# Performance work log

Hardware: AMD Instinct MI355X
Metric: run time of the kernel (lower is better)

## Reference

```python
import jax, jax.numpy as jnp
import numpy as np

STRIDE = 1
PAD = 1
KH = KW = 3


def _conv2d(x, w, b, stride, pad):
    out = jax.lax.conv_general_dilated(
        x, w, window_strides=(stride, stride),
        padding=[(pad, pad), (pad, pad)],
        dimension_numbers=("NCHW", "OIHW", "NCHW"))
    return out + b[None, :, None, None]


def _deform_conv2d(x, offset, mask, weight, stride, pad):
    """Modulated deformable conv v2 (torchvision deform_conv2d semantics, no bias).

    x: [B,C,H,W]  offset: [B,2*K2,Ho,Wo] (dy,dx interleaved per tap)
    mask: [B,K2,Ho,Wo]  weight: [O,C,KH,KW]
    """
    B, C, H, W = x.shape
    O = weight.shape[0]
    K2 = KH * KW
    Ho, Wo = offset.shape[2], offset.shape[3]

    dy = offset[:, 0::2]  # [B,K2,Ho,Wo]
    dx = offset[:, 1::2]

    # base sampling grid per kernel tap k = i*KW + j
    ki = jnp.repeat(jnp.arange(KH), KW)  # [K2]
    kj = jnp.tile(jnp.arange(KW), KH)    # [K2]
    base_y = (jnp.arange(Ho) * stride - pad)[None, :, None] + ki[:, None, None]  # [K2,Ho,1]
    base_x = (jnp.arange(Wo) * stride - pad)[None, None, :] + kj[:, None, None]  # [K2,1,Wo]

    py = base_y[None].astype(x.dtype) + dy  # [B,K2,Ho,Wo]
    px = base_x[None].astype(x.dtype) + dx

    y0f = jnp.floor(py)
    x0f = jnp.floor(px)
    wy = py - y0f  # bilinear weights
    wx = px - x0f
    y0 = y0f.astype(jnp.int32)
    x0 = x0f.astype(jnp.int32)

    x_flat = x.reshape(B, C, H * W)

    def gather(yi, xi):
        # zero padding: out-of-range integer neighbors contribute 0
        valid = (yi >= 0) & (yi < H) & (xi >= 0) & (xi < W)
        idx = jnp.clip(yi, 0, H - 1) * W + jnp.clip(xi, 0, W - 1)  # [B,K2,Ho,Wo]
        g = jax.vmap(lambda xf, id_: xf[:, id_])(x_flat, idx)      # [B,C,K2,Ho,Wo]
        return g * valid[:, None].astype(x.dtype)

    v00 = gather(y0, x0)
    v01 = gather(y0, x0 + 1)
    v10 = gather(y0 + 1, x0)
    v11 = gather(y0 + 1, x0 + 1)

    wy_ = wy[:, None]  # [B,1,K2,Ho,Wo]
    wx_ = wx[:, None]
    val = (v00 * (1 - wy_) * (1 - wx_) + v01 * (1 - wy_) * wx_
           + v10 * wy_ * (1 - wx_) + v11 * wy_ * wx_)
    val = val * mask[:, None]

    # conv accumulation over (C, K2)
    return jnp.einsum("bckhw,ock->bohw", val, weight.reshape(O, C, K2))


def setup_inputs() -> dict:
    key = jax.random.key(0)
    ks = jax.random.split(key, 6)
    B, C, O, H, W = 4, 128, 128, 64, 64
    x = jax.random.normal(ks[0], (B, C, H, W), dtype=jnp.float32)
    org_w = jax.random.normal(ks[1], (O, C, KH, KW), dtype=jnp.float32) * 0.05
    offset_w = jax.random.normal(ks[2], (2 * KH * KW, C, 3, 3), dtype=jnp.float32) * 0.01
    offset_b = jax.random.normal(ks[3], (2 * KH * KW,), dtype=jnp.float32) * 0.01
    mask_w = jax.random.normal(ks[4], (KH * KW, C, 3, 3), dtype=jnp.float32) * 0.01
    mask_b = jax.random.normal(ks[5], (KH * KW,), dtype=jnp.float32) * 0.01
    return {"x": x, "org_w": org_w, "offset_w": offset_w, "offset_b": offset_b,
            "mask_w": mask_w, "mask_b": mask_b}


def reference(x, org_w, offset_w, offset_b, mask_w, mask_b):
    offset = _conv2d(x, offset_w, offset_b, STRIDE, 1)          # [B,18,H,W]
    mask = jax.nn.sigmoid(_conv2d(x, mask_w, mask_b, STRIDE, 1))  # [B,9,H,W]
    return _deform_conv2d(x, offset, mask, org_w, STRIDE, PAD)
```

## Files before the change

kernel.cpp:

```cpp
#include <hip/hip_runtime.h>
#include <hip/hip_bf16.h>
#include <cmath>

#define B_    4
#define C_    128
#define O_    128
#define K2T   9
#define CK    1152
#define NPIX  4096
#define ROWS  7
#define BUFC  448
#define BUFV  (16 * BUFC)
#define NGRP  36

using bf16   = __bf16;
using bf16x8 = __attribute__((ext_vector_type(8))) __bf16;
using f32x4  = __attribute__((ext_vector_type(4))) float;

#define WS_WBF 0
#define WS_WOM 294912

__global__ void __launch_bounds__(256) repack_kernel(
    const float* __restrict__ org_w, const float* __restrict__ offset_w,
    const float* __restrict__ mask_w, bf16* __restrict__ w_bf,
    bf16* __restrict__ wom_bf) {
  int t = blockIdx.x * 256 + threadIdx.x;
  if (t >= 160 * CK) return;
  int row = t / CK, r = t % CK;
  int cc = r / 288, rr = r % 288;
  int k = rr >> 5, cq = rr & 31;
  int c = cc * 32 + cq;
  if (row < 128) {
    w_bf[t] = (bf16)org_w[((size_t)row * C_ + c) * K2T + k];
  } else {
    int ch = row - 128;
    float v = 0.f;
    if (ch < 18)      v = offset_w[((size_t)ch * C_ + c) * K2T + k];
    else if (ch < 27) v = mask_w[((size_t)(ch - 18) * C_ + c) * K2T + k];
    wom_bf[(size_t)ch * CK + r] = (bf16)v;
  }
}

__device__ __forceinline__ void gl_lds16(const float* src, float* lds_uniform) {
  __builtin_amdgcn_global_load_lds(
      (const __attribute__((address_space(1))) void*)src,
      (__attribute__((address_space(3))) void*)lds_uniform, 16, 0, 0);
}

__global__ void __launch_bounds__(576) deform_fused_kernel(
    const float* __restrict__ x, const bf16* __restrict__ w_bf,
    const bf16* __restrict__ wom_bf, const float* __restrict__ off_b,
    const float* __restrict__ mask_b, float* __restrict__ out) {
  __shared__ __align__(16) float xslab[4 * BUFV];
  __shared__ __align__(16) bf16  valbuf[NGRP * 512];
  __shared__ __align__(16) float S_lds[32 * 64];

  int tid  = threadIdx.x;
  int bid0 = blockIdx.x;
  int bid  = (bid0 & 7) * 32 + (bid0 >> 3);
  int b    = bid >> 6, ho = bid & 63;
  int lane = tid & 63, wv = tid >> 6;
  int l15  = lane & 15, l4 = lane >> 4;
  bool w8  = (wv < 8);

  const float* xb = x + (size_t)b * C_ * NPIX;

  auto stage = [&](int t) {
    if (w8 && t < 16) {
      int chbase = (t & 7) * 16;
      float* bufb = xslab + (size_t)(t & 3) * BUFV;
#pragma unroll
      for (int u = 0; u < 2; ++u) {
        int chl = 2 * wv + u;
        const float* srcc = xb + (size_t)(chbase + chl) * NPIX + l15 * 4;
        float* dst = bufb + chl * BUFC;
        if (t < 8) {
          int y = ho - 1 + l4; y = y < 0 ? 0 : (y > 63 ? 63 : y);
          gl_lds16(srcc + y * 64, dst + 128);
        } else {
          int ya = ho - 3 + l4; ya = ya < 0 ? 0 : (ya > 63 ? 63 : ya);
          int yb = ho + l4;     yb = yb < 0 ? 0 : (yb > 63 ? 63 : yb);
          gl_lds16(srcc + ya * 64, dst);
          gl_lds16(srcc + yb * 64, dst + 192);
        }
      }
    }
  };

  float apw; int apsa;
  {
    int ki = wv / 3, kj = wv % 3;
    int row = ho - 1 + ki, colu = lane - 1 + kj;
    bool ok = ((unsigned)row < 64u) && ((unsigned)colu < 64u);
    int ccl = colu < 0 ? 0 : (colu > 63 ? 63 : colu);
    apw  = ok ? 1.f : 0.f;
    apsa = (ki + 2) * 64 + ccl;
  }

  stage(0); stage(1); stage(2); stage(3);
  __builtin_amdgcn_sched_barrier(0);

  f32x4 acc1 = {};
  f32x4 acc[4] = {};
  bf16x8 aF[9];
  float pw0 = 0.f, pw1 = 0.f, pw2 = 0.f, pw3 = 0.f;
  int   psa = 0, psb = 0;
  int   mf1 = wv & 1, nfq1 = wv >> 1;
  const bf16* wb1 = wom_bf + (size_t)(mf1 * 16 + l15) * CK + l4 * 8;
  const bf16* wb  = w_bf  + (size_t)(wv * 16 + l15) * CK + l4 * 8;
  const bf16* vr1 = valbuf + l4 * 512 + (nfq1 * 16 + (l15 ^ l4)) * 8;
  const bf16* vrB = valbuf + l4 * 512 + (l15 ^ l4) * 8;

#pragma unroll 1
  for (int p = 0; p < 8; ++p) {
    bool passB = (p >= 4);
    int cc = p & 3;
    if (p == 7)      asm volatile("s_waitcnt vmcnt(0)" ::: "memory");
    else if (p < 3)  asm volatile("s_waitcnt vmcnt(4)" ::: "memory");
    else             asm volatile("s_waitcnt vmcnt(8)" ::: "memory");
    __builtin_amdgcn_s_barrier();
    __builtin_amdgcn_sched_barrier(0);
    if (w8) {
      const bf16* ab = (passB ? wb : wb1) + cc * 288;
#pragma unroll
      for (int ks = 0; ks < 9; ++ks) aF[ks] = *(const bf16x8*)(ab + ks * 32);
      __builtin_amdgcn_sched_barrier(0);
    }
    {
      const float* bufA = xslab + (size_t)((2 * p) & 3) * BUFV;
      const float* bufB2 = xslab + (size_t)((2 * p + 1) & 3) * BUFV;
#pragma unroll
      for (int q = 0; q < 4; ++q) {
        const float* bb = (q < 2) ? bufA : bufB2;
        int h = q & 1;
        bf16x8 pack;
        if (passB) {
#pragma unroll
          for (int j = 0; j < 8; ++j) {
            const float* cb = bb + (h * 8 + j) * BUFC;
            float a0 = cb[psa], a1 = cb[psa + 64];
            float b0 = cb[psb], b1 = cb[psb + 64];
            pack[j] = (bf16)(pw0 * a0 + pw1 * b0 + pw2 * a1 + pw3 * b1);
          }
        } else {
#pragma unroll
          for (int j = 0; j < 8; ++j)
            pack[j] = (bf16)(apw * bb[(h * 8 + j) * BUFC + apsa]);
        }
        *(bf16x8*)(valbuf + (wv * 4 + q) * 512 + (lane ^ q) * 8) = pack;
      }
    }
    asm volatile("s_waitcnt lgkmcnt(0)" ::: "memory");
    __builtin_amdgcn_s_barrier();
    __builtin_amdgcn_sched_barrier(0);
    stage(2 * p + 4); stage(2 * p + 5);
    __builtin_amdgcn_sched_barrier(0);
    if (w8) {
      __builtin_amdgcn_s_setprio(1);
      if (passB) {
#pragma unroll
        for (int ks = 0; ks < 9; ++ks) {
#pragma unroll
          for (int nf = 0; nf < 4; ++nf) {
            bf16x8 bv = *(const bf16x8*)(vrB + ks * 2048 + nf * 128);
            acc[nf] = __builtin_amdgcn_mfma_f32_16x16x32_bf16(aF[ks], bv, acc[nf], 0, 0, 0);
          }
        }
      } else {
#pragma unroll
        for (int ks = 0; ks < 9; ++ks) {
          bf16x8 bv = *(const bf16x8*)(vr1 + ks * 2048);
          acc1 = __builtin_amdgcn_mfma_f32_16x16x32_bf16(aF[ks], bv, acc1, 0, 0, 0);
        }
      }
      __builtin_amdgcn_s_setprio(0);
    }
    if (p == 3) {
      if (w8) {
        int so = mf1 * 16 + l4 * 4;
        int sp = nfq1 * 16 + l15;
#pragma unroll
        for (int r = 0; r < 4; ++r) S_lds[(so + r) * 64 + sp] = acc1[r];
      }
      asm volatile("s_waitcnt lgkmcnt(0)" ::: "memory");
      __builtin_amdgcn_s_barrier();
      __builtin_amdgcn_sched_barrier(0);
      {
        int k = wv, pp = lane;
        float dy = S_lds[(2 * k) * 64 + pp]     + off_b[2 * k];
        float dx = S_lds[(2 * k + 1) * 64 + pp] + off_b[2 * k + 1];
        float mz = S_lds[(18 + k) * 64 + pp]    + mask_b[k];
        float m  = 1.f / (1.f + expf(-mz));
        int ki = k / 3, kj = k % 3;
        float py = (float)(ho - 1 + ki) + dy;
        float px = (float)(pp - 1 + kj) + dx;
        float fy = floorf(py), fx = floorf(px);
        int y0 = (int)fy, x0 = (int)fx;
        float wy = py - fy, wx = px - fx;
        float vy0 = ((unsigned)y0       < 64u) ? 1.f : 0.f;
        float vy1 = ((unsigned)(y0 + 1) < 64u) ? 1.f : 0.f;
        float vx0 = ((unsigned)x0       < 64u) ? 1.f : 0.f;
        float vx1 = ((unsigned)(x0 + 1) < 64u) ? 1.f : 0.f;
        int r0  = y0 - (ho - 3);
        int ir0 = r0 < 0 ? 0 : (r0 > ROWS - 2 ? ROWS - 2 : r0);
        int c0  = x0 < 0 ? 0 : (x0 > 63 ? 63 : x0);
        int x1  = x0 + 1;
        int c1  = x1 < 0 ? 0 : (x1 > 63 ? 63 : x1);
        pw0 = (1.f - wy) * (1.f - wx) * m * vy0 * vx0;
        pw1 = (1.f - wy) * wx         * m * vy0 * vx1;
        pw2 = wy * (1.f - wx)         * m * vy1 * vx0;
        pw3 = wy * wx                 * m * vy1 * vx1;
        psa = ir0 * 64 + c0;
        psb = ir0 * 64 + c1;
      }
    }
  }

  if (w8) {
    float* ob = out + (size_t)b * O_ * NPIX + ho * 64;
#pragma unroll
    for (int nf = 0; nf < 4; ++nf)
#pragma unroll
      for (int r = 0; r < 4; ++r) {
        int o = wv * 16 + l4 * 4 + r;
        int pp = nf * 16 + l15;
        ob[(size_t)o * NPIX + pp] = acc[nf][r];
      }
  }
}

extern "C" void kernel_launch(void* const* d_in, const int* in_sizes, int n_in,
                              void* d_out, int out_size, void* d_ws, size_t ws_size,
                              hipStream_t stream) {
  const float* x        = (const float*)d_in[0];
  const float* org_w    = (const float*)d_in[1];
  const float* offset_w = (const float*)d_in[2];
  const float* off_b    = (const float*)d_in[3];
  const float* mask_w   = (const float*)d_in[4];
  const float* mask_b   = (const float*)d_in[5];
  float* out = (float*)d_out;
  char*  ws  = (char*)d_ws;

  bf16* w_bf   = (bf16*)(ws + WS_WBF);
  bf16* wom_bf = (bf16*)(ws + WS_WOM);

  repack_kernel<<<720, 256, 0, stream>>>(org_w, offset_w, mask_w, w_bf, wom_bf);
  deform_fused_kernel<<<256, 576, 0, stream>>>(x, w_bf, wom_bf, off_b, mask_b, out);
}
```

Measured before the change: 41.51 us.

## Load whole x window once into LDS as bf16 instead of streaming fp32 slabs

Replaces the pipelined global_load_lds staging of fp32 channel slabs (a four-buffer ring refilled each pass) with a single up-front load of all 128 channels × 7 rows, converted to bf16 in LDS. Per-pass vmcnt waits and restaging disappear, and the bilinear samples are read as bf16 and widened to fp32. The cost is a serialized prologue with per-element scalar loads and no overlap with compute, about 115 KB of LDS, and reduced precision of the sampled inputs, since the bf16 rounding now happens before interpolation.

```diff
diff --git a/kernel.cpp b/kernel.cpp
--- a/kernel.cpp
+++ b/kernel.cpp
@@ -9,8 +9,7 @@
 #define CK    1152
 #define NPIX  4096
 #define ROWS  7
-#define BUFC  448
-#define BUFV  (16 * BUFC)
+#define WCH   448
 #define NGRP  36
 
 using bf16   = __bf16;
@@ -41,17 +40,15 @@
   }
 }
 
-__device__ __forceinline__ void gl_lds16(const float* src, float* lds_uniform) {
-  __builtin_amdgcn_global_load_lds(
-      (const __attribute__((address_space(1))) void*)src,
-      (__attribute__((address_space(3))) void*)lds_uniform, 16, 0, 0);
+__device__ __forceinline__ float bf16_to_f32(unsigned short u) {
+  return __builtin_bit_cast(float, (unsigned)u << 16);
 }
 
 __global__ void __launch_bounds__(576) deform_fused_kernel(
     const float* __restrict__ x, const bf16* __restrict__ w_bf,
     const bf16* __restrict__ wom_bf, const float* __restrict__ off_b,
     const float* __restrict__ mask_b, float* __restrict__ out) {
-  __shared__ __align__(16) float xslab[4 * BUFV];
+  __shared__ __align__(16) unsigned short xw[128 * WCH];
   __shared__ __align__(16) bf16  valbuf[NGRP * 512];
   __shared__ __align__(16) float S_lds[32 * 64];
 
@@ -65,40 +62,25 @@
 
   const float* xb = x + (size_t)b * C_ * NPIX;
 
-  auto stage = [&](int t) {
-    if (w8 && t < 16) {
-      int chbase = (t & 7) * 16;
-      float* bufb = xslab + (size_t)(t & 3) * BUFV;
-#pragma unroll
-      for (int u = 0; u < 2; ++u) {
-        int chl = 2 * wv + u;
-        const float* srcc = xb + (size_t)(chbase + chl) * NPIX + l15 * 4;
-        float* dst = bufb + chl * BUFC;
-        if (t < 8) {
-          int y = ho - 1 + l4; y = y < 0 ? 0 : (y > 63 ? 63 : y);
-          gl_lds16(srcc + y * 64, dst + 128);
-        } else {
-          int ya = ho - 3 + l4; ya = ya < 0 ? 0 : (ya > 63 ? 63 : ya);
-          int yb = ho + l4;     yb = yb < 0 ? 0 : (yb > 63 ? 63 : yb);
-          gl_lds16(srcc + ya * 64, dst);
-          gl_lds16(srcc + yb * 64, dst + 192);
-        }
-      }
-    }
-  };
-
-  float apw; int apsa;
+  for (int rid = wv; rid < 896; rid += 9) {
+    int ch = rid / 7, r = rid - ch * 7;
+    int y = ho - 3 + r; y = y < 0 ? 0 : (y > 63 ? 63 : y);
+    float v = xb[(size_t)ch * NPIX + y * 64 + lane];
+    bf16 bv = (bf16)v;
+    xw[ch * WCH + r * 64 + lane] = __builtin_bit_cast(unsigned short, bv);
+  }
+  asm volatile("s_waitcnt lgkmcnt(0)" ::: "memory");
+  __builtin_amdgcn_s_barrier();
+  __builtin_amdgcn_sched_barrier(0);
+
+  bool apok; int apsa;
   {
     int ki = wv / 3, kj = wv % 3;
     int row = ho - 1 + ki, colu = lane - 1 + kj;
-    bool ok = ((unsigned)row < 64u) && ((unsigned)colu < 64u);
+    apok = ((unsigned)row < 64u) && ((unsigned)colu < 64u);
     int ccl = colu < 0 ? 0 : (colu > 63 ? 63 : colu);
-    apw  = ok ? 1.f : 0.f;
     apsa = (ki + 2) * 64 + ccl;
   }
-
-  stage(0); stage(1); stage(2); stage(3);
-  __builtin_amdgcn_sched_barrier(0);
 
   f32x4 acc1 = {};
   f32x4 acc[4] = {};
@@ -115,9 +97,6 @@
   for (int p = 0; p < 8; ++p) {
     bool passB = (p >= 4);
     int cc = p & 3;
-    if (p == 7)      asm volatile("s_waitcnt vmcnt(0)" ::: "memory");
-    else if (p < 3)  asm volatile("s_waitcnt vmcnt(4)" ::: "memory");
-    else             asm volatile("s_waitcnt vmcnt(8)" ::: "memory");
     __builtin_amdgcn_s_barrier();
     __builtin_amdgcn_sched_barrier(0);
     if (w8) {
@@ -127,33 +106,32 @@
       __builtin_amdgcn_sched_barrier(0);
     }
     {
-      const float* bufA = xslab + (size_t)((2 * p) & 3) * BUFV;
-      const float* bufB2 = xslab + (size_t)((2 * p + 1) & 3) * BUFV;
 #pragma unroll
       for (int q = 0; q < 4; ++q) {
-        const float* bb = (q < 2) ? bufA : bufB2;
-        int h = q & 1;
+        const unsigned short* cw = xw + (size_t)(cc * 32 + q * 8) * WCH;
         bf16x8 pack;
         if (passB) {
 #pragma unroll
           for (int j = 0; j < 8; ++j) {
-            const float* cb = bb + (h * 8 + j) * BUFC;
-            float a0 = cb[psa], a1 = cb[psa + 64];
-            float b0 = cb[psb], b1 = cb[psb + 64];
+            const unsigned short* c_ = cw + j * WCH;
+            float a0 = bf16_to_f32(c_[psa]);
+            float a1 = bf16_to_f32(c_[psa + 64]);
+            float b0 = bf16_to_f32(c_[psb]);
+            float b1 = bf16_to_f32(c_[psb + 64]);
             pack[j] = (bf16)(pw0 * a0 + pw1 * b0 + pw2 * a1 + pw3 * b1);
           }
         } else {
 #pragma unroll
-          for (int j = 0; j < 8; ++j)
-            pack[j] = (bf16)(apw * bb[(h * 8 + j) * BUFC + apsa]);
+          for (int j = 0; j < 8; ++j) {
+            float v = apok ? bf16_to_f32(cw[j * WCH + apsa]) : 0.f;
+            pack[j] = (bf16)v;
+          }
         }
         *(bf16x8*)(valbuf + (wv * 4 + q) * 512 + (lane ^ q) * 8) = pack;
       }
     }
     asm volatile("s_waitcnt lgkmcnt(0)" ::: "memory");
     __builtin_amdgcn_s_barrier();
-    __builtin_amdgcn_sched_barrier(0);
-    stage(2 * p + 4); stage(2 * p + 5);
     __builtin_amdgcn_sched_barrier(0);
     if (w8) {
       __builtin_amdgcn_s_setprio(1);
```

New measurement: 48.83 us. 1.18x slower.
